# Optimization experiments

Measured on AMD Instinct MI355X. Metric: run time of the kernel, lower is better.

The kernel has to match this reference:

```python
import jax, jax.numpy as jnp
import numpy as np

B, T, DIN, H, L = 32, 1024, 768, 768, 4  # batch, seq, dim_in, dim_u, num_layers


def _gru_layer(x, W_ih, W_hh, b_ih, b_hh):
    """PyTorch-semantics single-layer GRU, batch_first, h0=0.
    x: [B,T,D]; W_ih: [3H,D]; W_hh: [3H,H]; b_ih,b_hh: [3H]. Returns [B,T,H]."""
    Bn = x.shape[0]
    Hn = W_hh.shape[1]
    # precompute input contributions for all timesteps in one big GEMM
    xg = jnp.einsum('btd,gd->btg', x, W_ih) + b_ih  # [B,T,3H]

    def step(h, xg_t):
        hg = h @ W_hh.T + b_hh                      # [B,3H]
        xr, xz, xn = jnp.split(xg_t, 3, axis=-1)
        hr, hz, hn = jnp.split(hg, 3, axis=-1)
        r = jax.nn.sigmoid(xr + hr)
        z = jax.nn.sigmoid(xz + hz)
        n = jnp.tanh(xn + r * hn)
        h_new = (1.0 - z) * n + z * h
        return h_new, h_new

    h0 = jnp.zeros((Bn, Hn), x.dtype)
    _, ys = jax.lax.scan(step, h0, jnp.swapaxes(xg, 0, 1))  # scan over T
    return jnp.swapaxes(ys, 0, 1)                            # [B,T,H]


def setup_inputs() -> dict:
    key = jax.random.key(0)
    ks = jax.random.split(key, 10)
    s = 1.0 / np.sqrt(H)  # PyTorch GRU default init scale
    u = lambda k, shp: jax.random.uniform(k, shp, jnp.float32, -s, s)
    return {
        "x": jax.random.normal(ks[0], (B, T, DIN), jnp.float32),
        # first layer (dim_in -> dim_u)
        "W_ih0": u(ks[1], (3 * H, DIN)),
        "W_hh0": u(ks[2], (3 * H, H)),
        "b_ih0": u(ks[3], (3 * H,)),
        "b_hh0": u(ks[4], (3 * H,)),
        # remaining L-1 layers (dim_u -> dim_u), stacked
        "W_ih_s": u(ks[5], (L - 1, 3 * H, H)),
        "W_hh_s": u(ks[6], (L - 1, 3 * H, H)),
        "b_ih_s": u(ks[7], (L - 1, 3 * H)),
        "b_hh_s": u(ks[8], (L - 1, 3 * H)),
    }


def reference(x, W_ih0, W_hh0, b_ih0, b_hh0, W_ih_s, W_hh_s, b_ih_s, b_hh_s):
    out = _gru_layer(x, W_ih0, W_hh0, b_ih0, b_hh0)
    for i in range(L - 1):
        flipped = out[:, ::-1, :]  # reverse along time, per-layer direction flip
        out = flipped + _gru_layer(flipped, W_ih_s[i], W_hh_s[i], b_ih_s[i], b_hh_s[i])
    return out[:, ::-1, :]        # final reverse (matches torch code exactly)
```

## Files before the change

kernel.cpp:

```cpp
#include <hip/hip_runtime.h>
#include <hip/hip_bf16.h>
#include <stdint.h>

#define T_LEN 1024
#define NBATCH 32
#define HDIM 768
#define G3 2304
#define NBLK 48

typedef __attribute__((ext_vector_type(8))) short short8;
typedef __attribute__((ext_vector_type(4))) float f32x4;
typedef unsigned long long u64;

__device__ __forceinline__ unsigned short f2bf(float f) {
  union { float f; unsigned u; } v; v.f = f;
  return (unsigned short)((v.u + 0x7FFFu + ((v.u >> 16) & 1u)) >> 16);
}
__device__ __forceinline__ float bf2f(unsigned hs) {
  union { unsigned u; float f; } v; v.u = hs << 16; return v.f;
}
__device__ __forceinline__ unsigned pack2(float a, float b) {
  return (unsigned)f2bf(a) | ((unsigned)f2bf(b) << 16);
}
__device__ __forceinline__ float sigm(float x) {
  return __fdividef(1.f, 1.f + __expf(-x));
}
__device__ __forceinline__ float ftanh(float x) {
  return 1.f - __fdividef(2.f, __expf(2.f * x) + 1.f);
}

__global__ __launch_bounds__(256) void gemm_xg(
    const float* __restrict__ src, const float* __restrict__ W,
    const float* __restrict__ b_ih, const float* __restrict__ b_hh,
    unsigned short* __restrict__ xg, int flip)
{
  __shared__ unsigned short As[128 * 40];
  __shared__ unsigned short Bs[128 * 40];

  const int bx = blockIdx.x % 18;
  const int by = blockIdx.x / 18;
  const int tid = threadIdx.x;
  const int lane = tid & 63;
  const int w = tid >> 6;
  const int wm = w & 1, wn = w >> 1;

  f32x4 acc[4][4];
#pragma unroll
  for (int i = 0; i < 4; i++)
#pragma unroll
    for (int j = 0; j < 4; j++) acc[i][j] = (f32x4){0.f, 0.f, 0.f, 0.f};

  const int r = tid >> 1;
  const int ch = (tid & 1) * 16;

  const int m = by * 128 + r;
  const int tt = m >> 5, bb = m & 31;
  const int srow = flip ? (bb * T_LEN + (T_LEN - 1 - tt)) : (bb * T_LEN + tt);
  const float* arow = src + (size_t)srow * HDIM;
  const int gn = bx * 128 + r;
  const float* brow = W + (size_t)gn * HDIM;

  for (int k0 = 0; k0 < HDIM; k0 += 32) {
    {
      const float4* pa = (const float4*)(arow + k0 + ch);
      float4 a0 = pa[0], a1 = pa[1], a2 = pa[2], a3 = pa[3];
      uint4 q0, q1;
      q0.x = pack2(a0.x, a0.y); q0.y = pack2(a0.z, a0.w);
      q0.z = pack2(a1.x, a1.y); q0.w = pack2(a1.z, a1.w);
      q1.x = pack2(a2.x, a2.y); q1.y = pack2(a2.z, a2.w);
      q1.z = pack2(a3.x, a3.y); q1.w = pack2(a3.z, a3.w);
      *(uint4*)&As[r * 40 + ch] = q0;
      *(uint4*)&As[r * 40 + ch + 8] = q1;

      const float4* pb = (const float4*)(brow + k0 + ch);
      float4 b0 = pb[0], b1 = pb[1], b2 = pb[2], b3 = pb[3];
      q0.x = pack2(b0.x, b0.y); q0.y = pack2(b0.z, b0.w);
      q0.z = pack2(b1.x, b1.y); q0.w = pack2(b1.z, b1.w);
      q1.x = pack2(b2.x, b2.y); q1.y = pack2(b2.z, b2.w);
      q1.z = pack2(b3.x, b3.y); q1.w = pack2(b3.z, b3.w);
      *(uint4*)&Bs[r * 40 + ch] = q0;
      *(uint4*)&Bs[r * 40 + ch + 8] = q1;
    }
    __syncthreads();

    short8 af[4], bfv[4];
    const int kk = (lane >> 4) * 8;
#pragma unroll
    for (int i = 0; i < 4; i++)
      af[i] = *(const short8*)&As[(wm * 64 + i * 16 + (lane & 15)) * 40 + kk];
#pragma unroll
    for (int j = 0; j < 4; j++)
      bfv[j] = *(const short8*)&Bs[(wn * 64 + j * 16 + (lane & 15)) * 40 + kk];
#pragma unroll
    for (int i = 0; i < 4; i++)
#pragma unroll
      for (int j = 0; j < 4; j++)
        acc[i][j] = __builtin_amdgcn_mfma_f32_16x16x32_bf16(af[i], bfv[j], acc[i][j], 0, 0, 0);
    __syncthreads();
  }

#pragma unroll
  for (int j = 0; j < 4; j++) {
    const int g = bx * 128 + wn * 64 + j * 16 + (lane & 15);
    const float bias = b_ih[g] + (g < 1536 ? b_hh[g] : 0.f);
#pragma unroll
    for (int i = 0; i < 4; i++) {
      const int mrow = by * 128 + wm * 64 + i * 16 + (lane >> 4) * 4;
#pragma unroll
      for (int e = 0; e < 4; e++)
        xg[(size_t)(mrow + e) * G3 + g] = f2bf(acc[i][j][e] + bias);
    }
  }
}

__global__ __launch_bounds__(256, 1) void gru_scan(
    const unsigned short* __restrict__ xg,
    const float* __restrict__ Whh,
    const float* __restrict__ bhh,
    const float* __restrict__ res_src,
    float* __restrict__ outp,
    unsigned* __restrict__ hglob,
    unsigned* __restrict__ flags,
    int add_res, int final_flip)
{
  extern __shared__ unsigned short Wl[];
  __shared__ float hgbuf[4][3][32][17];
  __shared__ float bhn_s[16];

  const int tid = threadIdx.x;
  const int lane = tid & 63;
  const int w = tid >> 6;
  const int J0 = blockIdx.x * 16;

  for (int idx = tid; idx < 48 * 96; idx += 256) {
    const int rr = idx / 96;
    const int c8 = (idx % 96) * 8;
    const int g = rr >> 4, j = rr & 15;
    const float* p = Whh + (size_t)(g * HDIM + J0 + j) * HDIM + c8;
    float4 v0 = *(const float4*)p;
    float4 v1 = *(const float4*)(p + 4);
    uint4 q;
    q.x = pack2(v0.x, v0.y); q.y = pack2(v0.z, v0.w);
    q.z = pack2(v1.x, v1.y); q.w = pack2(v1.z, v1.w);
    *(uint4*)&Wl[rr * 776 + c8] = q;
  }
  if (tid < 16) bhn_s[tid] = bhh[1536 + J0 + tid];
  __syncthreads();

  const int ub = (tid * 2) >> 4;
  const int uj = (tid * 2) & 15;
  float h_old0 = 0.f, h_old1 = 0.f;

  unsigned pxr, pxz, pxn;
  float2 pres = make_float2(0.f, 0.f);
  {
    const size_t base = (size_t)(0 * 32 + ub) * G3 + J0 + uj;
    pxr = *(const unsigned*)(xg + base);
    pxz = *(const unsigned*)(xg + base + 768);
    pxn = *(const unsigned*)(xg + base + 1536);
    if (add_res)
      pres = *(const float2*)(res_src + ((size_t)ub * T_LEN + (T_LEN - 1)) * HDIM + J0 + uj);
  }

  const u64* __restrict__ hq = (const u64*)hglob;

  for (int t = 0; t < T_LEN; ++t) {
    if (t > 0) {
      const unsigned want = (unsigned)t;
      for (;;) {
        unsigned f = 0xFFFFFFFFu;
        if (lane < NBLK)
          f = __hip_atomic_load(&flags[lane], __ATOMIC_RELAXED, __HIP_MEMORY_SCOPE_AGENT);
        if (__all((int)(f >= want))) break;
      }
      asm volatile("" ::: "memory");
    }

    const u64* hb = hq + (size_t)(t & 1) * (NBATCH * HDIM / 4);

    u64 h0q[6][2], h1q[6][2];
#pragma unroll
    for (int kk = 0; kk < 6; ++kk) {
      const int k0 = (w * 6 + kk) * 32 + (lane >> 4) * 8;
      const int qi0 = (lane & 15) * 192 + (k0 >> 2);
      const int qi1 = qi0 + 16 * 192;
      h0q[kk][0] = __hip_atomic_load(&hb[qi0],     __ATOMIC_RELAXED, __HIP_MEMORY_SCOPE_AGENT);
      h0q[kk][1] = __hip_atomic_load(&hb[qi0 + 1], __ATOMIC_RELAXED, __HIP_MEMORY_SCOPE_AGENT);
      h1q[kk][0] = __hip_atomic_load(&hb[qi1],     __ATOMIC_RELAXED, __HIP_MEMORY_SCOPE_AGENT);
      h1q[kk][1] = __hip_atomic_load(&hb[qi1 + 1], __ATOMIC_RELAXED, __HIP_MEMORY_SCOPE_AGENT);
    }

    f32x4 acc[3][2];
#pragma unroll
    for (int g = 0; g < 3; g++)
#pragma unroll
      for (int mt = 0; mt < 2; mt++) acc[g][mt] = (f32x4){0.f, 0.f, 0.f, 0.f};

#pragma unroll
    for (int kk = 0; kk < 6; ++kk) {
      const int k0 = (w * 6 + kk) * 32 + (lane >> 4) * 8;
      union { u64 q[2]; short8 s; } ua0, ua1;
      ua0.q[0] = h0q[kk][0]; ua0.q[1] = h0q[kk][1];
      ua1.q[0] = h1q[kk][0]; ua1.q[1] = h1q[kk][1];
#pragma unroll
      for (int g = 0; g < 3; ++g) {
        short8 bfr = *(const short8*)&Wl[(g * 16 + (lane & 15)) * 776 + k0];
        acc[g][0] = __builtin_amdgcn_mfma_f32_16x16x32_bf16(ua0.s, bfr, acc[g][0], 0, 0, 0);
        acc[g][1] = __builtin_amdgcn_mfma_f32_16x16x32_bf16(ua1.s, bfr, acc[g][1], 0, 0, 0);
      }
    }

#pragma unroll
    for (int g = 0; g < 3; ++g)
#pragma unroll
      for (int mt = 0; mt < 2; ++mt)
#pragma unroll
        for (int e = 0; e < 4; ++e)
          hgbuf[w][g][mt * 16 + (lane >> 4) * 4 + e][lane & 15] = acc[g][mt][e];
    __syncthreads();

    const float hr0 = hgbuf[0][0][ub][uj] + hgbuf[1][0][ub][uj] + hgbuf[2][0][ub][uj] + hgbuf[3][0][ub][uj];
    const float hz0 = hgbuf[0][1][ub][uj] + hgbuf[1][1][ub][uj] + hgbuf[2][1][ub][uj] + hgbuf[3][1][ub][uj];
    const float hn0 = hgbuf[0][2][ub][uj] + hgbuf[1][2][ub][uj] + hgbuf[2][2][ub][uj] + hgbuf[3][2][ub][uj];
    const float hr1 = hgbuf[0][0][ub][uj+1] + hgbuf[1][0][ub][uj+1] + hgbuf[2][0][ub][uj+1] + hgbuf[3][0][ub][uj+1];
    const float hz1 = hgbuf[0][1][ub][uj+1] + hgbuf[1][1][ub][uj+1] + hgbuf[2][1][ub][uj+1] + hgbuf[3][1][ub][uj+1];
    const float hn1 = hgbuf[0][2][ub][uj+1] + hgbuf[1][2][ub][uj+1] + hgbuf[2][2][ub][uj+1] + hgbuf[3][2][ub][uj+1];

    const float r0 = sigm(bf2f(pxr & 0xffffu) + hr0);
    const float z0 = sigm(bf2f(pxz & 0xffffu) + hz0);
    const float n0 = ftanh(bf2f(pxn & 0xffffu) + r0 * (hn0 + bhn_s[uj]));
    const float r1 = sigm(bf2f(pxr >> 16) + hr1);
    const float z1 = sigm(bf2f(pxz >> 16) + hz1);
    const float n1 = ftanh(bf2f(pxn >> 16) + r1 * (hn1 + bhn_s[uj + 1]));
    const float hnew0 = (1.f - z0) * n0 + z0 * h_old0;
    const float hnew1 = (1.f - z1) * n1 + z1 * h_old1;
    h_old0 = hnew0; h_old1 = hnew1;

    unsigned* hnb = hglob + (size_t)((t + 1) & 1) * (NBATCH * HDIM / 2);
    __hip_atomic_store(&hnb[ub * 384 + ((J0 + uj) >> 1)], pack2(hnew0, hnew1),
                       __ATOMIC_RELAXED, __HIP_MEMORY_SCOPE_AGENT);
    asm volatile("s_waitcnt vmcnt(0)" ::: "memory");
    __syncthreads();
    if (tid == 0)
      __hip_atomic_store(&flags[blockIdx.x], (unsigned)(t + 1),
                         __ATOMIC_RELAXED, __HIP_MEMORY_SCOPE_AGENT);

    const float o0 = hnew0 + (add_res ? pres.x : 0.f);
    const float o1 = hnew1 + (add_res ? pres.y : 0.f);
    const size_t orow = final_flip ? ((size_t)ub * T_LEN + (T_LEN - 1 - t))
                                   : ((size_t)ub * T_LEN + t);
    *(float2*)(outp + orow * HDIM + J0 + uj) = make_float2(o0, o1);

    if (t + 1 < T_LEN) {
      const size_t base = ((size_t)(t + 1) * 32 + ub) * G3 + J0 + uj;
      pxr = *(const unsigned*)(xg + base);
      pxz = *(const unsigned*)(xg + base + 768);
      pxn = *(const unsigned*)(xg + base + 1536);
      if (add_res)
        pres = *(const float2*)(res_src + ((size_t)ub * T_LEN + (T_LEN - 2 - t)) * HDIM + J0 + uj);
    }
  }
}

extern "C" void kernel_launch(void* const* d_in, const int* in_sizes, int n_in,
                              void* d_out, int out_size, void* d_ws, size_t ws_size,
                              hipStream_t stream) {
  const float* x      = (const float*)d_in[0];
  const float* W_ih0  = (const float*)d_in[1];
  const float* W_hh0  = (const float*)d_in[2];
  const float* b_ih0  = (const float*)d_in[3];
  const float* b_hh0  = (const float*)d_in[4];
  const float* W_ih_s = (const float*)d_in[5];
  const float* W_hh_s = (const float*)d_in[6];
  const float* b_ih_s = (const float*)d_in[7];
  const float* b_hh_s = (const float*)d_in[8];
  float* out = (float*)d_out;

  char* ws = (char*)d_ws;
  size_t off = 0;
  auto alloc = [&](size_t bytes) -> void* {
    void* p = ws + off; off += (bytes + 255) & ~(size_t)255; return p;
  };
  unsigned short* xg = (unsigned short*)alloc((size_t)T_LEN * 32 * G3 * 2);
  float* buf0 = (float*)alloc((size_t)32 * T_LEN * HDIM * 4);
  float* buf1 = (float*)alloc((size_t)32 * T_LEN * HDIM * 4);
  unsigned* hglob = (unsigned*)alloc(2 * NBATCH * HDIM * 2);
  unsigned* flags = (unsigned*)alloc(64 * 4);

  hipFuncSetAttribute((const void*)gru_scan,
                      hipFuncAttributeMaxDynamicSharedMemorySize, 48 * 776 * 2);

  for (int l = 0; l < 4; ++l) {
    const float* src = (l == 0) ? x : ((l == 2) ? buf1 : buf0);
    float* dst = (l == 3) ? out : ((l == 1) ? buf1 : buf0);
    const float* Wih = (l == 0) ? W_ih0 : W_ih_s + (size_t)(l - 1) * G3 * HDIM;
    const float* Whh = (l == 0) ? W_hh0 : W_hh_s + (size_t)(l - 1) * G3 * HDIM;
    const float* bih = (l == 0) ? b_ih0 : b_ih_s + (size_t)(l - 1) * G3;
    const float* bhh = (l == 0) ? b_hh0 : b_hh_s + (size_t)(l - 1) * G3;

    hipMemsetAsync(hglob, 0, 2 * NBATCH * HDIM * 2, stream);
    hipMemsetAsync(flags, 0, 64 * 4, stream);

    gemm_xg<<<dim3(18 * 256), dim3(256), 0, stream>>>(src, Wih, bih, bhh, xg, l > 0 ? 1 : 0);

    gru_scan<<<dim3(NBLK), dim3(256), 48 * 776 * 2, stream>>>(
        xg, Whh, bhh, (l > 0) ? src : nullptr, dst, hglob, flags,
        l > 0 ? 1 : 0, l == 3 ? 1 : 0);
  }
}
```

Baseline: 23.59 ms.

## Replace per-step flag barrier with sentinel-polled per-timestep hidden-state slots

The cross-block synchronization no longer uses per-block step flags. Each timestep's hidden state gets its own slot, pre-filled with 0xFFFF sentinel values, and consumers poll the h data directly until no sentinel remains. This removes the store-wait, the extra __syncthreads and the flag store/poll round trip on the serial critical path. The shared reduction buffer is double-buffered to avoid a WAR hazard now that the second barrier is gone. The cost is a roughly 50MB memset per layer to fill the sentinels, and the scheme relies on 64-bit atomic loads never observing a torn or partial write. It also assumes a bf16 hidden value never equals 0xFFFF, which is a NaN pattern.

```diff
diff --git a/kernel.cpp b/kernel.cpp
--- a/kernel.cpp
+++ b/kernel.cpp
@@ -119,12 +119,11 @@
     const float* __restrict__ bhh,
     const float* __restrict__ res_src,
     float* __restrict__ outp,
-    unsigned* __restrict__ hglob,
-    unsigned* __restrict__ flags,
+    unsigned* __restrict__ hseq,
     int add_res, int final_flip)
 {
   extern __shared__ unsigned short Wl[];
-  __shared__ float hgbuf[4][3][32][17];
+  __shared__ float hgbuf[2][4][3][32][17];
   __shared__ float bhn_s[16];
 
   const int tid = threadIdx.x;
@@ -162,32 +161,37 @@
       pres = *(const float2*)(res_src + ((size_t)ub * T_LEN + (T_LEN - 1)) * HDIM + J0 + uj);
   }
 
-  const u64* __restrict__ hq = (const u64*)hglob;
+  const u64* __restrict__ hq = (const u64*)hseq;
+
+  int qbase[6];
+#pragma unroll
+  for (int kk = 0; kk < 6; ++kk) {
+    const int k0 = (w * 6 + kk) * 32 + (lane >> 4) * 8;
+    qbase[kk] = (lane & 15) * 192 + (k0 >> 2);
+  }
 
   for (int t = 0; t < T_LEN; ++t) {
-    if (t > 0) {
-      const unsigned want = (unsigned)t;
-      for (;;) {
-        unsigned f = 0xFFFFFFFFu;
-        if (lane < NBLK)
-          f = __hip_atomic_load(&flags[lane], __ATOMIC_RELAXED, __HIP_MEMORY_SCOPE_AGENT);
-        if (__all((int)(f >= want))) break;
+    const u64* hb = hq + (size_t)t * (NBATCH * HDIM / 4);
+
+    u64 hv[6][4];
+    for (;;) {
+#pragma unroll
+      for (int kk = 0; kk < 6; ++kk) {
+        hv[kk][0] = __hip_atomic_load(&hb[qbase[kk]],            __ATOMIC_RELAXED, __HIP_MEMORY_SCOPE_AGENT);
+        hv[kk][1] = __hip_atomic_load(&hb[qbase[kk] + 1],        __ATOMIC_RELAXED, __HIP_MEMORY_SCOPE_AGENT);
+        hv[kk][2] = __hip_atomic_load(&hb[qbase[kk] + 16 * 192],     __ATOMIC_RELAXED, __HIP_MEMORY_SCOPE_AGENT);
+        hv[kk][3] = __hip_atomic_load(&hb[qbase[kk] + 16 * 192 + 1], __ATOMIC_RELAXED, __HIP_MEMORY_SCOPE_AGENT);
       }
-      asm volatile("" ::: "memory");
-    }
-
-    const u64* hb = hq + (size_t)(t & 1) * (NBATCH * HDIM / 4);
-
-    u64 h0q[6][2], h1q[6][2];
-#pragma unroll
-    for (int kk = 0; kk < 6; ++kk) {
-      const int k0 = (w * 6 + kk) * 32 + (lane >> 4) * 8;
-      const int qi0 = (lane & 15) * 192 + (k0 >> 2);
-      const int qi1 = qi0 + 16 * 192;
-      h0q[kk][0] = __hip_atomic_load(&hb[qi0],     __ATOMIC_RELAXED, __HIP_MEMORY_SCOPE_AGENT);
-      h0q[kk][1] = __hip_atomic_load(&hb[qi0 + 1], __ATOMIC_RELAXED, __HIP_MEMORY_SCOPE_AGENT);
-      h1q[kk][0] = __hip_atomic_load(&hb[qi1],     __ATOMIC_RELAXED, __HIP_MEMORY_SCOPE_AGENT);
-      h1q[kk][1] = __hip_atomic_load(&hb[qi1 + 1], __ATOMIC_RELAXED, __HIP_MEMORY_SCOPE_AGENT);
+      unsigned stale = 0;
+#pragma unroll
+      for (int kk = 0; kk < 6; ++kk)
+#pragma unroll
+        for (int q = 0; q < 4; ++q) {
+          const u64 v = hv[kk][q];
+          stale |= (((unsigned)(v >> 16) & 0xFFFFu) == 0xFFFFu);
+          stale |= ((unsigned)(v >> 48) == 0xFFFFu);
+        }
+      if (!__any((int)stale)) break;
     }
 
     f32x4 acc[3][2];
@@ -200,8 +204,8 @@
     for (int kk = 0; kk < 6; ++kk) {
       const int k0 = (w * 6 + kk) * 32 + (lane >> 4) * 8;
       union { u64 q[2]; short8 s; } ua0, ua1;
-      ua0.q[0] = h0q[kk][0]; ua0.q[1] = h0q[kk][1];
-      ua1.q[0] = h1q[kk][0]; ua1.q[1] = h1q[kk][1];
+      ua0.q[0] = hv[kk][0]; ua0.q[1] = hv[kk][1];
+      ua1.q[0] = hv[kk][2]; ua1.q[1] = hv[kk][3];
 #pragma unroll
       for (int g = 0; g < 3; ++g) {
         short8 bfr = *(const short8*)&Wl[(g * 16 + (lane & 15)) * 776 + k0];
@@ -210,21 +214,22 @@
       }
     }
 
+    const int par = t & 1;
 #pragma unroll
     for (int g = 0; g < 3; ++g)
 #pragma unroll
       for (int mt = 0; mt < 2; ++mt)
 #pragma unroll
         for (int e = 0; e < 4; ++e)
-          hgbuf[w][g][mt * 16 + (lane >> 4) * 4 + e][lane & 15] = acc[g][mt][e];
+          hgbuf[par][w][g][mt * 16 + (lane >> 4) * 4 + e][lane & 15] = acc[g][mt][e];
     __syncthreads();
 
-    const float hr0 = hgbuf[0][0][ub][uj] + hgbuf[1][0][ub][uj] + hgbuf[2][0][ub][uj] + hgbuf[3][0][ub][uj];
-    const float hz0 = hgbuf[0][1][ub][uj] + hgbuf[1][1][ub][uj] + hgbuf[2][1][ub][uj] + hgbuf[3][1][ub][uj];
-    const float hn0 = hgbuf[0][2][ub][uj] + hgbuf[1][2][ub][uj] + hgbuf[2][2][ub][uj] + hgbuf[3][2][ub][uj];
-    const float hr1 = hgbuf[0][0][ub][uj+1] + hgbuf[1][0][ub][uj+1] + hgbuf[2][0][ub][uj+1] + hgbuf[3][0][ub][uj+1];
-    const float hz1 = hgbuf[0][1][ub][uj+1] + hgbuf[1][1][ub][uj+1] + hgbuf[2][1][ub][uj+1] + hgbuf[3][1][ub][uj+1];
-    const float hn1 = hgbuf[0][2][ub][uj+1] + hgbuf[1][2][ub][uj+1] + hgbuf[2][2][ub][uj+1] + hgbuf[3][2][ub][uj+1];
+    const float hr0 = hgbuf[par][0][0][ub][uj] + hgbuf[par][1][0][ub][uj] + hgbuf[par][2][0][ub][uj] + hgbuf[par][3][0][ub][uj];
+    const float hz0 = hgbuf[par][0][1][ub][uj] + hgbuf[par][1][1][ub][uj] + hgbuf[par][2][1][ub][uj] + hgbuf[par][3][1][ub][uj];
+    const float hn0 = hgbuf[par][0][2][ub][uj] + hgbuf[par][1][2][ub][uj] + hgbuf[par][2][2][ub][uj] + hgbuf[par][3][2][ub][uj];
+    const float hr1 = hgbuf[par][0][0][ub][uj+1] + hgbuf[par][1][0][ub][uj+1] + hgbuf[par][2][0][ub][uj+1] + hgbuf[par][3][0][ub][uj+1];
+    const float hz1 = hgbuf[par][0][1][ub][uj+1] + hgbuf[par][1][1][ub][uj+1] + hgbuf[par][2][1][ub][uj+1] + hgbuf[par][3][1][ub][uj+1];
+    const float hn1 = hgbuf[par][0][2][ub][uj+1] + hgbuf[par][1][2][ub][uj+1] + hgbuf[par][2][2][ub][uj+1] + hgbuf[par][3][2][ub][uj+1];
 
     const float r0 = sigm(bf2f(pxr & 0xffffu) + hr0);
     const float z0 = sigm(bf2f(pxz & 0xffffu) + hz0);
@@ -236,14 +241,9 @@
     const float hnew1 = (1.f - z1) * n1 + z1 * h_old1;
     h_old0 = hnew0; h_old1 = hnew1;
 
-    unsigned* hnb = hglob + (size_t)((t + 1) & 1) * (NBATCH * HDIM / 2);
-    __hip_atomic_store(&hnb[ub * 384 + ((J0 + uj) >> 1)], pack2(hnew0, hnew1),
+    __hip_atomic_store(&hseq[(size_t)(t + 1) * (NBATCH * HDIM / 2) + ub * 384 + ((J0 + uj) >> 1)],
+                       pack2(hnew0, hnew1),
                        __ATOMIC_RELAXED, __HIP_MEMORY_SCOPE_AGENT);
-    asm volatile("s_waitcnt vmcnt(0)" ::: "memory");
-    __syncthreads();
-    if (tid == 0)
-      __hip_atomic_store(&flags[blockIdx.x], (unsigned)(t + 1),
-                         __ATOMIC_RELAXED, __HIP_MEMORY_SCOPE_AGENT);
 
     const float o0 = hnew0 + (add_res ? pres.x : 0.f);
     const float o1 = hnew1 + (add_res ? pres.y : 0.f);
@@ -283,28 +283,27 @@
   };
   unsigned short* xg = (unsigned short*)alloc((size_t)T_LEN * 32 * G3 * 2);
   float* buf0 = (float*)alloc((size_t)32 * T_LEN * HDIM * 4);
-  float* buf1 = (float*)alloc((size_t)32 * T_LEN * HDIM * 4);
-  unsigned* hglob = (unsigned*)alloc(2 * NBATCH * HDIM * 2);
-  unsigned* flags = (unsigned*)alloc(64 * 4);
+  const size_t slot_bytes = (size_t)NBATCH * HDIM * 2;
+  unsigned* hseq = (unsigned*)alloc((size_t)(T_LEN + 1) * slot_bytes);
 
   hipFuncSetAttribute((const void*)gru_scan,
                       hipFuncAttributeMaxDynamicSharedMemorySize, 48 * 776 * 2);
 
   for (int l = 0; l < 4; ++l) {
-    const float* src = (l == 0) ? x : ((l == 2) ? buf1 : buf0);
-    float* dst = (l == 3) ? out : ((l == 1) ? buf1 : buf0);
+    const float* src = (l == 0) ? x : ((l == 2) ? buf0 : out);
+    float* dst = (l == 1) ? buf0 : out;
     const float* Wih = (l == 0) ? W_ih0 : W_ih_s + (size_t)(l - 1) * G3 * HDIM;
     const float* Whh = (l == 0) ? W_hh0 : W_hh_s + (size_t)(l - 1) * G3 * HDIM;
     const float* bih = (l == 0) ? b_ih0 : b_ih_s + (size_t)(l - 1) * G3;
     const float* bhh = (l == 0) ? b_hh0 : b_hh_s + (size_t)(l - 1) * G3;
 
-    hipMemsetAsync(hglob, 0, 2 * NBATCH * HDIM * 2, stream);
-    hipMemsetAsync(flags, 0, 64 * 4, stream);
+    hipMemsetAsync(hseq, 0, slot_bytes, stream);
+    hipMemsetAsync((char*)hseq + slot_bytes, 0xFF, (size_t)T_LEN * slot_bytes, stream);
 
     gemm_xg<<<dim3(18 * 256), dim3(256), 0, stream>>>(src, Wih, bih, bhh, xg, l > 0 ? 1 : 0);
 
     gru_scan<<<dim3(NBLK), dim3(256), 48 * 776 * 2, stream>>>(
-        xg, Whh, bhh, (l > 0) ? src : nullptr, dst, hglob, flags,
+        xg, Whh, bhh, (l > 0) ? src : nullptr, dst, hseq,
         l > 0 ? 1 : 0, l == 3 ? 1 : 0);
   }
 }
```

Measured after the change: 23.97 ms. No clear change (+1.7%).
